# Kernel tuning notes

Hardware: AMD Instinct MI355X
Metric: run time of the kernel (lower is better)

Reference implementation:

```python
import jax, jax.numpy as jnp
import numpy as np

WIDTH = 768
HEAD = 64

def setup_inputs() -> dict:
    key = jax.random.key(0)
    ks = jax.random.split(key, 8)
    x = jax.random.normal(ks[0], (8, 2048, WIDTH), dtype=jnp.float32)
    mask = jax.random.randint(ks[1], (2048, 2048), 0, 2, dtype=jnp.int32)
    s = 1.0 / np.sqrt(WIDTH)
    Wq = jax.random.normal(ks[2], (WIDTH, HEAD), dtype=jnp.float32) * s
    Wk = jax.random.normal(ks[3], (WIDTH, HEAD), dtype=jnp.float32) * s
    Wv = jax.random.normal(ks[4], (WIDTH, HEAD), dtype=jnp.float32) * s
    bq = jax.random.normal(ks[5], (HEAD,), dtype=jnp.float32) * 0.01
    bk = jax.random.normal(ks[6], (HEAD,), dtype=jnp.float32) * 0.01
    bv = jax.random.normal(ks[7], (HEAD,), dtype=jnp.float32) * 0.01
    return {"x": x, "Wq": Wq, "bq": bq, "Wk": Wk, "bk": bk, "Wv": Wv, "bv": bv, "mask": mask}

def reference(x, Wq, bq, Wk, bk, Wv, bv, mask) -> jnp.ndarray:
    # x: [B, N, width]; projections -> [B, N, head]
    Q = jnp.einsum('bnw,wh->bnh', x, Wq) + bq
    K = jnp.einsum('bnw,wh->bnh', x, Wk) + bk
    V = jnp.einsum('bnw,wh->bnh', x, Wv) + bv
    scale = 1.0 / jnp.sqrt(jnp.asarray(Q.shape[-1], dtype=Q.dtype))
    scores = jnp.einsum('bqh,bkh->bqk', Q, K) * scale  # [B, N, N]
    scores = jnp.where(mask == 0, -jnp.inf, scores)
    attn = jax.nn.softmax(scores, axis=-1)
    return jnp.einsum('bqk,bkh->bqh', attn, V)
```

## Files before the change

### kernel.cpp

```cpp
#include <hip/hip_runtime.h>

typedef short  s8v   __attribute__((ext_vector_type(8)));
typedef float  f32x4 __attribute__((ext_vector_type(4)));

#define SEQ 2048
#define WID 768

__device__ __forceinline__ unsigned fbits(float f) {
    union { float f; unsigned u; } v; v.f = f; return v.u;
}
__device__ __forceinline__ float bitsf(unsigned u) {
    union { unsigned u; float f; } v; v.u = u; return v.f;
}
__device__ __forceinline__ unsigned short f2b(float f) {
    unsigned u = fbits(f);
    return (unsigned short)((u + 0x7FFFu + ((u >> 16) & 1u)) >> 16);
}
__device__ __forceinline__ unsigned packRNE(float a, float b) {
    unsigned ta = fbits(a) + 0x7FFFu + ((fbits(a) >> 16) & 1u);
    unsigned tb = fbits(b) + 0x7FFFu + ((fbits(b) >> 16) & 1u);
    return __builtin_amdgcn_perm(tb, ta, 0x07060302u);
}
__device__ __forceinline__ unsigned packTRUNC(float a, float b) {
    return __builtin_amdgcn_perm(fbits(b), fbits(a), 0x07060302u);
}
__device__ __forceinline__ f32x4 zero4() { f32x4 z = {0.f, 0.f, 0.f, 0.f}; return z; }

__device__ __forceinline__ void async16(const unsigned short* g, unsigned short* l) {
    __builtin_amdgcn_global_load_lds(
        (const __attribute__((address_space(1))) unsigned int*)g,
        (__attribute__((address_space(3))) unsigned int*)l, 16, 0, 0);
}

__global__ __launch_bounds__(256) void convert_kernel(
    const int* __restrict__ mask,
    const float* __restrict__ Wq, const float* __restrict__ Wk, const float* __restrict__ Wv,
    unsigned short* __restrict__ WF, unsigned* __restrict__ PM)
{
    const int tid = threadIdx.x;
    const int blk = blockIdx.x;
    if (blk < 512) {
        const int gid  = blk * 4 + (tid >> 6);
        const int lane = tid & 63, quad = lane >> 4, c = lane & 15;
        const int qb = gid >> 5, kb = gid & 31;
        unsigned w = 0;
        #pragma unroll
        for (int mt = 0; mt < 2; ++mt) {
            const int q = qb * 32 + mt * 16 + c;
            #pragma unroll
            for (int i = 0; i < 4; ++i) {
                const int4 mm = *(const int4*)&mask[(size_t)q * SEQ + kb * 64 + quad * 16 + 4 * i];
                if (mm.x) w |= 1u << (mt * 16 + i * 4 + 0);
                if (mm.y) w |= 1u << (mt * 16 + i * 4 + 1);
                if (mm.z) w |= 1u << (mt * 16 + i * 4 + 2);
                if (mm.w) w |= 1u << (mt * 16 + i * 4 + 3);
            }
        }
        PM[(size_t)gid * 64 + lane] = w;
    } else {
        const int s2 = (blk - 512) * 256 + tid;
        const int chunk = s2 >> 6, l = s2 & 63;
        const int ntg = chunk / 24, r = chunk - ntg * 24;
        const int kc = r >> 1, h = r & 1;
        const int mat = ntg >> 2;
        const int col = (ntg & 3) * 16 + (l & 15);
        const int k0 = kc * 64 + h * 32 + (l >> 4) * 8;
        const float* Wm = (mat == 0) ? Wq : (mat == 1) ? Wk : Wv;
        float p[8];
        #pragma unroll
        for (int j = 0; j < 8; ++j) p[j] = Wm[(size_t)(k0 + j) * 64 + col];
        uint4 w;
        w.x = packRNE(p[0], p[1]); w.y = packRNE(p[2], p[3]);
        w.z = packRNE(p[4], p[5]); w.w = packRNE(p[6], p[7]);
        *(uint4*)&WF[(size_t)s2 * 8] = w;
    }
}

__global__ __launch_bounds__(512, 4) void qkv_proj_kernel(
    const float* __restrict__ x, const unsigned short* __restrict__ WF,
    const float* __restrict__ bq, const float* __restrict__ bk, const float* __restrict__ bv,
    unsigned short* __restrict__ QF, unsigned short* __restrict__ KF,
    unsigned short* __restrict__ VF)
{
    __shared__ unsigned short AB[2][16384];
    unsigned short (*St)[200] = (unsigned short(*)[200])AB;

    const int tid = threadIdx.x;
    const int wv = tid >> 6, lane = tid & 63, quad = lane >> 4, c = lane & 15;
    const int rg = wv >> 2, cg = wv & 3;
    const int blk = blockIdx.x;
    const int bsw = blk & 7, tsw = blk >> 3;
    const int kbt = bsw * 32 + tsw;
    const int g0  = kbt * 4;

    float bias[3];
    #pragma unroll
    for (int nt = 0; nt < 3; ++nt) {
        int col = cg * 48 + nt * 16 + c;
        const float* B = (col < 64) ? bq : (col < 128) ? bk : bv;
        bias[nt] = B[col & 63];
    }

    const int chunk = tid >> 6;
    const int gl = chunk >> 1, hh = chunk & 1;
    const int arow = (g0 + gl) * 16 + (lane & 15);
    const float* xrow = x + (size_t)arow * WID + hh * 32 + ((lane >> 4) & 3) * 8;

    auto issueB = [&](int kc, int b) {
        #pragma unroll
        for (int r = 0; r < 3; ++r) {
            const int e = wv * 3 + r;
            const int ntg = e >> 1, h = e & 1;
            async16(WF + (((size_t)ntg * 12 + kc) * 2 + h) * 512 + lane * 8,
                    &AB[b][4096 + (ntg * 2 + h) * 512]);
        }
    };
    auto stageA_write = [&](int b, float4 f0, float4 f1) {
        uint4 w;
        w.x = packRNE(f0.x, f0.y); w.y = packRNE(f0.z, f0.w);
        w.z = packRNE(f1.x, f1.y); w.w = packRNE(f1.z, f1.w);
        *(uint4*)&AB[b][(size_t)tid * 8] = w;
    };

    f32x4 acc[2][3];
    #pragma unroll
    for (int mt = 0; mt < 2; ++mt)
        #pragma unroll
        for (int nt = 0; nt < 3; ++nt) acc[mt][nt] = zero4();

    {
        float4 f0 = *(const float4*)&xrow[0];
        float4 f1 = *(const float4*)&xrow[4];
        stageA_write(0, f0, f1);
        issueB(0, 0);
    }

    for (int kc = 0; kc < 12; ++kc) {
        const int b = kc & 1;
        __syncthreads();
        float4 f0, f1;
        if (kc < 11) {
            f0 = *(const float4*)&xrow[(kc + 1) * 64];
            f1 = *(const float4*)&xrow[(kc + 1) * 64 + 4];
            issueB(kc + 1, b ^ 1);
        }

        s8v afr[2][2], bfr[3][2];
        #pragma unroll
        for (int mt = 0; mt < 2; ++mt)
            #pragma unroll
            for (int h = 0; h < 2; ++h)
                afr[mt][h] = *(const s8v*)&AB[b][((rg * 2 + mt) * 2 + h) * 512 + lane * 8];
        #pragma unroll
        for (int nt = 0; nt < 3; ++nt)
            #pragma unroll
            for (int h = 0; h < 2; ++h)
                bfr[nt][h] = *(const s8v*)&AB[b][4096 + ((cg * 3 + nt) * 2 + h) * 512 + lane * 8];
        #pragma unroll
        for (int h = 0; h < 2; ++h)
            #pragma unroll
            for (int mt = 0; mt < 2; ++mt)
                #pragma unroll
                for (int nt = 0; nt < 3; ++nt)
                    acc[mt][nt] = __builtin_amdgcn_mfma_f32_16x16x32_bf16(
                        afr[mt][h], bfr[nt][h], acc[mt][nt], 0, 0, 0);

        if (kc < 11) stageA_write(b ^ 1, f0, f1);
    }

    #pragma unroll
    for (int mt = 0; mt < 2; ++mt)
        #pragma unroll
        for (int nt = 0; nt < 3; ++nt)
            #pragma unroll
            for (int i = 0; i < 4; ++i)
                St[rg * 32 + mt * 16 + quad * 4 + i][cg * 48 + nt * 16 + c]
                    = f2b(acc[mt][nt][i] + bias[nt]);
    __syncthreads();

    {
        const int g = tid >> 7, ks = (tid >> 6) & 1, l = tid & 63;
        uint4 v = *(uint4*)&St[g * 16 + (l & 15)][ks * 32 + (l >> 4) * 8];
        *(uint4*)&QF[(((size_t)(g0 + g)) * 2 + ks) * 512 + (size_t)l * 8] = v;
    }
    {
        const int ksnt = tid >> 6, l = tid & 63;
        const int ks = ksnt >> 2, nt = ksnt & 3;
        uint4 v = *(uint4*)&St[4 * (l & 15) + nt][64 + ks * 32 + (l >> 4) * 8];
        *(uint4*)&KF[(((size_t)kbt * 8 + ksnt) * 64 + l) * 8] = v;
    }
    {
        const int ksnt = tid >> 6, l = tid & 63;
        const int ks = ksnt >> 2, nt = ksnt & 3;
        const int d = 128 + nt * 16 + (l & 15);
        const int r0 = (l >> 4) * 16 + ks * 8;
        unsigned short p[8];
        #pragma unroll
        for (int s = 0; s < 8; ++s) p[s] = St[r0 + s][d];
        uint4 w;
        w.x = (unsigned)p[0] | ((unsigned)p[1] << 16);
        w.y = (unsigned)p[2] | ((unsigned)p[3] << 16);
        w.z = (unsigned)p[4] | ((unsigned)p[5] << 16);
        w.w = (unsigned)p[6] | ((unsigned)p[7] << 16);
        *(uint4*)&VF[(((size_t)kbt * 8 + ksnt) * 64 + l) * 8] = w;
    }
}

__global__ __launch_bounds__(1024, 4) void attn_kernel(
    const unsigned short* __restrict__ QF, const unsigned short* __restrict__ KF,
    const unsigned short* __restrict__ VF, const unsigned* __restrict__ PM,
    float* __restrict__ out)
{
    __shared__ float Obuf[64][68];
    __shared__ float Lbuf[64];

    const int tid = threadIdx.x;
    const int wv = tid >> 6, lane = tid & 63, quad = lane >> 4, c = lane & 15;
    const int sl = wv & 3, qg = wv >> 2, mt = qg & 1;
    const int blk = blockIdx.x;
    const int bb = blk & 7, qt = blk >> 3;
    const size_t qrow0 = (size_t)bb * SEQ + qt * 64;

    if (tid < 64) Lbuf[tid] = 0.f;

    union Q8 { s8v v; unsigned w[4]; };
    Q8 qf[2];
    {
        const size_t qgrp = (size_t)bb * 128 + qt * 4 + qg;
        #pragma unroll
        for (int ks = 0; ks < 2; ++ks)
            qf[ks].v = *(const s8v*)&QF[(qgrp * 2 + ks) * 512 + (size_t)lane * 8];
    }

    f32x4 O[4];
    float lro0 = 0.f, lro1 = 0.f;
    #pragma unroll
    for (int nt = 0; nt < 4; ++nt) O[nt] = zero4();

    const unsigned* pmrow = PM + (size_t)((qt * 2 + (qg >> 1)) * 32 + sl * 8) * 64 + lane;

    #pragma unroll 1
    for (int kt = 0; kt < 8; ++kt) {
        const size_t kbg = (size_t)bb * 32 + sl * 8 + kt;
        const unsigned short* kb_ = KF + kbg * 4096 + (size_t)lane * 8;
        const unsigned short* vb_ = VF + kbg * 4096 + (size_t)lane * 8;

        const unsigned pmw = pmrow[(size_t)kt * 64];

        Q8 kf8[8], vf8[8];
        #pragma unroll
        for (int d = 0; d < 8; ++d) kf8[d].v = *(const s8v*)&kb_[(size_t)d * 512];
        #pragma unroll
        for (int d = 0; d < 8; ++d) vf8[d].v = *(const s8v*)&vb_[(size_t)d * 512];

        asm volatile("s_waitcnt vmcnt(8)" ::: "memory");
        #pragma unroll
        for (int d = 0; d < 8; ++d)
            #pragma unroll
            for (int j = 0; j < 4; ++j) asm volatile("" : "+v"(kf8[d].w[j]));
        __builtin_amdgcn_sched_barrier(0);

        f32x4 S[4];
        #pragma unroll
        for (int nt = 0; nt < 4; ++nt) S[nt] = zero4();
        #pragma unroll
        for (int ks = 0; ks < 2; ++ks)
            #pragma unroll
            for (int nt = 0; nt < 4; ++nt)
                S[nt] = __builtin_amdgcn_mfma_f32_16x16x32_bf16(kf8[ks * 4 + nt].v, qf[ks].v, S[nt], 0, 0, 0);

        const unsigned pmh = pmw >> (mt * 16);
        float p[4][4];
        #pragma unroll
        for (int i = 0; i < 4; ++i)
            #pragma unroll
            for (int nt = 0; nt < 4; ++nt) {
                float e = __builtin_amdgcn_exp2f(
                    fmaf(S[nt][i], 0.18033688011112042f, -21.640425613334451f));
                p[nt][i] = ((pmh >> (i * 4 + nt)) & 1u) ? e : 0.f;
            }
        union { unsigned w[8]; s8v v[2]; } P;
        #pragma unroll
        for (int j = 0; j < 8; ++j) {
            unsigned uu = packTRUNC(p[2 * (j & 1)][j >> 1], p[2 * (j & 1) + 1][j >> 1]);
            P.w[j] = uu;
            if (j & 1) lro1 += bitsf(uu << 16) + bitsf(uu & 0xFFFF0000u);
            else       lro0 += bitsf(uu << 16) + bitsf(uu & 0xFFFF0000u);
        }

        asm volatile("s_waitcnt vmcnt(0)" ::: "memory");
        #pragma unroll
        for (int d = 0; d < 8; ++d)
            #pragma unroll
            for (int j = 0; j < 4; ++j) asm volatile("" : "+v"(vf8[d].w[j]));
        __builtin_amdgcn_sched_barrier(0);

        #pragma unroll
        for (int ks = 0; ks < 2; ++ks)
            #pragma unroll
            for (int nt = 0; nt < 4; ++nt)
                O[nt] = __builtin_amdgcn_mfma_f32_16x16x32_bf16(P.v[ks], vf8[ks * 4 + nt].v, O[nt], 0, 0, 0);
    }

    #pragma unroll
    for (int j = 0; j < 5; ++j) {
        int idx = tid + 1024 * j;
        if (idx < 64 * 68) ((float*)Obuf)[idx] = 0.f;
    }
    __syncthreads();

    {
        float l = lro0 + lro1;
        l += __shfl_xor(l, 16);
        l += __shfl_xor(l, 32);
        if (quad == 0) atomicAdd(&Lbuf[qg * 16 + c], l);
    }
    #pragma unroll
    for (int i = 0; i < 4; ++i)
        #pragma unroll
        for (int nt = 0; nt < 4; ++nt)
            atomicAdd(&Obuf[qg * 16 + quad * 4 + i][nt * 16 + c], O[nt][i]);
    __syncthreads();
    {
        const int r = tid >> 4, d4 = (tid & 15) * 4;
        const float invL = 1.0f / Lbuf[r];
        float4 v = *(float4*)&Obuf[r][d4];
        float4 o = make_float4(v.x * invL, v.y * invL, v.z * invL, v.w * invL);
        *(float4*)&out[(qrow0 + r) * 64 + d4] = o;
    }
}

extern "C" void kernel_launch(void* const* d_in, const int* in_sizes, int n_in,
                              void* d_out, int out_size, void* d_ws, size_t ws_size,
                              hipStream_t stream)
{
    const float* x    = (const float*)d_in[0];
    const float* Wq   = (const float*)d_in[1];
    const float* bq   = (const float*)d_in[2];
    const float* Wk   = (const float*)d_in[3];
    const float* bk   = (const float*)d_in[4];
    const float* Wv   = (const float*)d_in[5];
    const float* bv   = (const float*)d_in[6];
    const int*   mask = (const int*)d_in[7];
    float* out = (float*)d_out;

    unsigned short* QF = (unsigned short*)d_ws;
    unsigned short* KF = QF + (size_t)16384 * 64;
    unsigned short* VF = KF + (size_t)16384 * 64;
    unsigned short* WF = VF + (size_t)16384 * 64;
    unsigned*       PM = (unsigned*)(WF + (size_t)192 * WID);

    convert_kernel<<<584, 256, 0, stream>>>(mask, Wq, Wk, Wv, WF, PM);
    qkv_proj_kernel<<<256, 512, 0, stream>>>(x, WF, bq, bk, bv, QF, KF, VF);
    attn_kernel<<<256, 1024, 0, stream>>>(QF, KF, VF, PM, out);
}
```

Baseline: 159.7 us.

## Halve QKV projection row tile to launch twice as many blocks

The QKV projection kernel now processes 32 rows per block instead of 64, doubling the grid from 256 to 512 blocks. Each warp computes one M tile instead of two, the A staging buffer shrinks, and the K/V fragment write-out is remapped so each block fills half of a key tile's layout. The aim is better occupancy and latency hiding across the 256 CUs. The cost is that the weight tiles are reloaded by twice as many blocks and each block does less MFMA work per sync.

```diff
diff --git a/kernel.cpp b/kernel.cpp
--- a/kernel.cpp
+++ b/kernel.cpp
@@ -82,7 +82,7 @@
     unsigned short* __restrict__ QF, unsigned short* __restrict__ KF,
     unsigned short* __restrict__ VF)
 {
-    __shared__ unsigned short AB[2][16384];
+    __shared__ unsigned short AB[2][14336];
     unsigned short (*St)[200] = (unsigned short(*)[200])AB;
 
     const int tid = threadIdx.x;
@@ -90,8 +90,9 @@
     const int rg = wv >> 2, cg = wv & 3;
     const int blk = blockIdx.x;
     const int bsw = blk & 7, tsw = blk >> 3;
-    const int kbt = bsw * 32 + tsw;
-    const int g0  = kbt * 4;
+    const int kbt2 = bsw * 64 + tsw;
+    const int kbt  = kbt2 >> 1, hb = kbt2 & 1;
+    const int g0r  = kbt2 * 2;
 
     float bias[3];
     #pragma unroll
@@ -101,10 +102,12 @@
         bias[nt] = B[col & 63];
     }
 
-    const int chunk = tid >> 6;
-    const int gl = chunk >> 1, hh = chunk & 1;
-    const int arow = (g0 + gl) * 16 + (lane & 15);
-    const float* xrow = x + (size_t)arow * WID + hh * 32 + ((lane >> 4) & 3) * 8;
+    const int ach = tid >> 7;
+    const int agl = ach >> 1, ah = ach & 1;
+    const int al  = (tid >> 1) & 63;
+    const int aj0 = (tid & 1) * 4;
+    const float* xptr = x + (size_t)((g0r + agl) * 16 + (al & 15)) * WID
+                          + ah * 32 + ((al >> 4) & 3) * 8 + aj0;
 
     auto issueB = [&](int kc, int b) {
         #pragma unroll
@@ -112,88 +115,82 @@
             const int e = wv * 3 + r;
             const int ntg = e >> 1, h = e & 1;
             async16(WF + (((size_t)ntg * 12 + kc) * 2 + h) * 512 + lane * 8,
-                    &AB[b][4096 + (ntg * 2 + h) * 512]);
+                    &AB[b][2048 + (ntg * 2 + h) * 512]);
         }
     };
-    auto stageA_write = [&](int b, float4 f0, float4 f1) {
-        uint4 w;
-        w.x = packRNE(f0.x, f0.y); w.y = packRNE(f0.z, f0.w);
-        w.z = packRNE(f1.x, f1.y); w.w = packRNE(f1.z, f1.w);
-        *(uint4*)&AB[b][(size_t)tid * 8] = w;
+    auto stageA = [&](int b, float4 f) {
+        uint2 w2;
+        w2.x = packRNE(f.x, f.y);
+        w2.y = packRNE(f.z, f.w);
+        *(uint2*)&AB[b][(size_t)tid * 4] = w2;
     };
 
-    f32x4 acc[2][3];
-    #pragma unroll
-    for (int mt = 0; mt < 2; ++mt)
-        #pragma unroll
-        for (int nt = 0; nt < 3; ++nt) acc[mt][nt] = zero4();
+    f32x4 acc[3];
+    #pragma unroll
+    for (int nt = 0; nt < 3; ++nt) acc[nt] = zero4();
 
     {
-        float4 f0 = *(const float4*)&xrow[0];
-        float4 f1 = *(const float4*)&xrow[4];
-        stageA_write(0, f0, f1);
+        float4 f = *(const float4*)&xptr[0];
+        stageA(0, f);
         issueB(0, 0);
     }
 
     for (int kc = 0; kc < 12; ++kc) {
         const int b = kc & 1;
         __syncthreads();
-        float4 f0, f1;
+        float4 f;
         if (kc < 11) {
-            f0 = *(const float4*)&xrow[(kc + 1) * 64];
-            f1 = *(const float4*)&xrow[(kc + 1) * 64 + 4];
+            f = *(const float4*)&xptr[(kc + 1) * 64];
             issueB(kc + 1, b ^ 1);
         }
 
-        s8v afr[2][2], bfr[3][2];
-        #pragma unroll
-        for (int mt = 0; mt < 2; ++mt)
+        s8v afr[2], bfr[3][2];
+        #pragma unroll
+        for (int h = 0; h < 2; ++h)
+            afr[h] = *(const s8v*)&AB[b][(rg * 2 + h) * 512 + lane * 8];
+        #pragma unroll
+        for (int nt = 0; nt < 3; ++nt)
             #pragma unroll
             for (int h = 0; h < 2; ++h)
-                afr[mt][h] = *(const s8v*)&AB[b][((rg * 2 + mt) * 2 + h) * 512 + lane * 8];
-        #pragma unroll
-        for (int nt = 0; nt < 3; ++nt)
-            #pragma unroll
-            for (int h = 0; h < 2; ++h)
-                bfr[nt][h] = *(const s8v*)&AB[b][4096 + ((cg * 3 + nt) * 2 + h) * 512 + lane * 8];
+                bfr[nt][h] = *(const s8v*)&AB[b][2048 + ((cg * 3 + nt) * 2 + h) * 512 + lane * 8];
         #pragma unroll
         for (int h = 0; h < 2; ++h)
             #pragma unroll
-            for (int mt = 0; mt < 2; ++mt)
-                #pragma unroll
-                for (int nt = 0; nt < 3; ++nt)
-                    acc[mt][nt] = __builtin_amdgcn_mfma_f32_16x16x32_bf16(
-                        afr[mt][h], bfr[nt][h], acc[mt][nt], 0, 0, 0);
-
-        if (kc < 11) stageA_write(b ^ 1, f0, f1);
-    }
-
-    #pragma unroll
-    for (int mt = 0; mt < 2; ++mt)
-        #pragma unroll
-        for (int nt = 0; nt < 3; ++nt)
-            #pragma unroll
-            for (int i = 0; i < 4; ++i)
-                St[rg * 32 + mt * 16 + quad * 4 + i][cg * 48 + nt * 16 + c]
-                    = f2b(acc[mt][nt][i] + bias[nt]);
+            for (int nt = 0; nt < 3; ++nt)
+                acc[nt] = __builtin_amdgcn_mfma_f32_16x16x32_bf16(
+                    afr[h], bfr[nt][h], acc[nt], 0, 0, 0);
+
+        if (kc < 11) stageA(b ^ 1, f);
+    }
+
+    #pragma unroll
+    for (int nt = 0; nt < 3; ++nt)
+        #pragma unroll
+        for (int i = 0; i < 4; ++i)
+            St[rg * 16 + quad * 4 + i][cg * 48 + nt * 16 + c]
+                = f2b(acc[nt][i] + bias[nt]);
     __syncthreads();
 
-    {
+    if (tid < 256) {
         const int g = tid >> 7, ks = (tid >> 6) & 1, l = tid & 63;
         uint4 v = *(uint4*)&St[g * 16 + (l & 15)][ks * 32 + (l >> 4) * 8];
-        *(uint4*)&QF[(((size_t)(g0 + g)) * 2 + ks) * 512 + (size_t)l * 8] = v;
-    }
-    {
-        const int ksnt = tid >> 6, l = tid & 63;
+        *(uint4*)&QF[(((size_t)(g0r + g)) * 2 + ks) * 512 + (size_t)l * 8] = v;
+    } else {
+        const int t2 = tid - 256;
+        const int ksnt = t2 >> 5, idx = t2 & 31;
         const int ks = ksnt >> 2, nt = ksnt & 3;
-        uint4 v = *(uint4*)&St[4 * (l & 15) + nt][64 + ks * 32 + (l >> 4) * 8];
+        const int qd = idx >> 3, ci = idx & 7;
+        const int l = qd * 16 + hb * 8 + ci;
+        uint4 v = *(uint4*)&St[4 * ci + nt][64 + ks * 32 + qd * 8];
         *(uint4*)&KF[(((size_t)kbt * 8 + ksnt) * 64 + l) * 8] = v;
     }
-    {
-        const int ksnt = tid >> 6, l = tid & 63;
+    if (tid < 256) {
+        const int ksnt = tid >> 5, idx = tid & 31;
         const int ks = ksnt >> 2, nt = ksnt & 3;
-        const int d = 128 + nt * 16 + (l & 15);
-        const int r0 = (l >> 4) * 16 + ks * 8;
+        const int qd = hb * 2 + (idx >> 4), c2 = idx & 15;
+        const int l = qd * 16 + c2;
+        const int r0 = (idx >> 4) * 16 + ks * 8;
+        const int d = 128 + nt * 16 + c2;
         unsigned short p[8];
         #pragma unroll
         for (int s = 0; s < 8; ++s) p[s] = St[r0 + s][d];
@@ -351,6 +348,6 @@
     unsigned*       PM = (unsigned*)(WF + (size_t)192 * WID);
 
     convert_kernel<<<584, 256, 0, stream>>>(mask, Wq, Wk, Wv, WF, PM);
-    qkv_proj_kernel<<<256, 512, 0, stream>>>(x, WF, bq, bk, bv, QF, KF, VF);
+    qkv_proj_kernel<<<512, 512, 0, stream>>>(x, WF, bq, bk, bv, QF, KF, VF);
     attn_kernel<<<256, 1024, 0, stream>>>(QF, KF, VF, PM, out);
 }
```

Result: no change. 160.0 us (+0.2%).
